# Kernel tuning notes

Measured on AMD Instinct MI355X. Metric: run time of the kernel, lower is better.

## Reference

```python
import jax, jax.numpy as jnp
import numpy as np

R = 8          # num_real
P = 8          # num_complex_conjugate_pairs
L = 4          # num_layers (hidden Linear+ReLU blocks)
H = 256        # hidden_dim
B = 16384      # batch


def _init_params(key, C, out_dim):
    ks = jax.random.split(key, 6)
    s_in = 1.0  # fan_in = 1
    s_h = 1.0 / np.sqrt(H)
    return dict(
        W_in=jax.random.uniform(ks[0], (C, H), jnp.float32, -s_in, s_in),
        b_in=jax.random.uniform(ks[1], (C, H), jnp.float32, -s_in, s_in),
        W_h=jax.random.uniform(ks[2], (L, C, H, H), jnp.float32, -s_h, s_h),
        b_h=jax.random.uniform(ks[3], (L, C, H), jnp.float32, -s_h, s_h),
        W_out=jax.random.uniform(ks[4], (C, out_dim, H), jnp.float32, -s_h, s_h),
        b_out=jax.random.uniform(ks[5], (C, out_dim), jnp.float32, -s_h, s_h),
    )


def setup_inputs() -> dict:
    key = jax.random.key(0)
    kz, kr, kc = jax.random.split(key, 3)
    z = jax.random.normal(kz, (B, R + 2 * P), jnp.float32)
    pr = _init_params(kr, R, 1)   # real-eigenvalue MLPs, out_dim=1
    pc = _init_params(kc, P, 2)   # complex-pair MLPs, out_dim=2
    return {
        "z": z,
        "Wr_in": pr["W_in"], "br_in": pr["b_in"],
        "Wr_h": pr["W_h"], "br_h": pr["b_h"],
        "Wr_out": pr["W_out"], "br_out": pr["b_out"],
        "Wc_in": pc["W_in"], "bc_in": pc["b_in"],
        "Wc_h": pc["W_h"], "bc_h": pc["b_h"],
        "Wc_out": pc["W_out"], "bc_out": pc["b_out"],
    }


def _grouped_mlp(x, W_in, b_in, W_h, b_h, W_out, b_out):
    # x: [B, C] scalar input per channel; all C tiny MLPs run as grouped GEMMs.
    h = jax.nn.relu(x[..., None] * W_in + b_in)            # [B, C, H]
    for l in range(W_h.shape[0]):
        h = jax.nn.relu(jnp.einsum('bci,coi->bco', h, W_h[l]) + b_h[l])
    return jnp.einsum('bci,coi->bco', h, W_out) + b_out     # [B, C, out]


def reference(z, Wr_in, br_in, Wr_h, br_h, Wr_out, br_out,
              Wc_in, bc_in, Wc_h, bc_h, Wc_out, bc_out):
    # real channels: z[..., i] -> Linear chains -> real_lambda [B, R]
    real_lambda = _grouped_mlp(z[..., :R], Wr_in, br_in, Wr_h, br_h,
                               Wr_out, br_out)[..., 0]
    # complex pairs: magnitude z_r^2 + z_i^2 per pair -> (mu, omega)
    z_mag = z[..., R::2] ** 2 + z[..., R + 1::2] ** 2        # [B, P]
    mu_omega = _grouped_mlp(z_mag, Wc_in, bc_in, Wc_h, bc_h,
                            Wc_out, bc_out)                  # [B, P, 2]
    mu = mu_omega[..., 0]
    omega = mu_omega[..., 1]
    return real_lambda, mu, omega
```

## Files before the change

### kernel.cpp

```cpp
#include <hip/hip_runtime.h>

#define OUT_MU 131072
#define OUT_OM 262144
#define WOUT_OFF 4210688

typedef _Float16 half8 __attribute__((ext_vector_type(8)));
typedef __fp16   fp16x2 __attribute__((ext_vector_type(2)));
typedef float    floatx4 __attribute__((ext_vector_type(4)));
typedef unsigned uint2v __attribute__((ext_vector_type(2)));

__device__ __forceinline__ void wait_lgkm0() {
    asm volatile("s_waitcnt lgkmcnt(0)" ::: "memory");
}
__device__ __forceinline__ void wait_vm0() {
    asm volatile("s_waitcnt vmcnt(0)" ::: "memory");
}
__device__ __forceinline__ void barrier_raw() {
    asm volatile("s_barrier" ::: "memory");
}

#define AS1 __attribute__((address_space(1)))
#define AS3 __attribute__((address_space(3)))

__global__ void prep_w(const float* __restrict__ Wr_h,
                       const float* __restrict__ Wc_h,
                       _Float16* __restrict__ dst) {
    int v = blockIdx.x * 256 + threadIdx.x;
    int r16 = v & 15;
    int ks  = (v >> 4) & 3;
    int nt  = (v >> 6) & 3;
    int wv  = (v >> 8) & 3;
    int g   = (v >> 10) & 31;
    int ch  = v >> 15;
    int l = g >> 3, kk = g & 7;
    int n  = wv * 64 + nt * 16 + r16;
    int k0 = kk * 32 + ks * 8;
    const float* src = (ch < 8) ? Wr_h : Wc_h;
    int c = ch & 7;
    const float* p = src + ((size_t)((l * 8 + c) * 256 + n)) * 256 + k0;
    float4 a = *(const float4*)p;
    float4 b = *(const float4*)(p + 4);
    half8 o;
    o[0] = (_Float16)a.x; o[1] = (_Float16)a.y; o[2] = (_Float16)a.z; o[3] = (_Float16)a.w;
    o[4] = (_Float16)b.x; o[5] = (_Float16)b.y; o[6] = (_Float16)b.z; o[7] = (_Float16)b.w;
    *(half8*)(dst + (size_t)v * 8) = o;
}

__global__ void prep_wo(const float* __restrict__ Wr_out,
                        const float* __restrict__ Wc_out,
                        _Float16* __restrict__ dst) {
    int t = blockIdx.x * 256 + threadIdx.x;
    int j = t & 255, d = (t >> 8) & 1, ch = t >> 9;
    int c = ch & 7;
    float v;
    if (ch < 8) v = d ? 0.f : Wr_out[c * 256 + j];
    else        v = Wc_out[(c * 2 + d) * 256 + j];
    dst[WOUT_OFF + t] = (_Float16)v;
}

__global__ __launch_bounds__(256, 2)
void mlp_fused(const float* __restrict__ z,
               const float* __restrict__ Wr_in, const float* __restrict__ br_in,
               const float* __restrict__ Wc_in, const float* __restrict__ bc_in,
               const float* __restrict__ br_h,  const float* __restrict__ bc_h,
               const float* __restrict__ br_out, const float* __restrict__ bc_out,
               const _Float16* __restrict__ wst,
               float* __restrict__ out) {
    __shared__ __align__(16) char smem[77824];
    const int tid  = threadIdx.x;
    const int lane = tid & 63;
    const int wv   = tid >> 6;
    const int bid  = blockIdx.x;
    const int ch   = bid & 15;
    const int m0   = (bid >> 4) * 128;
    const bool isC = ch >= 8;
    const int c    = ch & 7;
    const int ks   = lane >> 4;
    const int r16  = lane & 15;
    float* zbuf = (float*)(smem + 65536);

    {
        const float* zs = z + (size_t)m0 * 24 + wv * 768 + lane * 4;
        char* zd = smem + 65536 + wv * 3072;
        __builtin_amdgcn_global_load_lds((const AS1 void*)zs,         (AS3 void*)zd,          16, 0, 0);
        __builtin_amdgcn_global_load_lds((const AS1 void*)(zs + 256), (AS3 void*)(zd + 1024), 16, 0, 0);
        __builtin_amdgcn_global_load_lds((const AS1 void*)(zs + 512), (AS3 void*)(zd + 2048), 16, 0, 0);
    }

    const half8* wl = (const half8*)wst + (size_t)ch * 32768 + wv * 256 + lane;

    half8 wr2[2][4];
    #pragma unroll
    for (int nt = 0; nt < 4; ++nt) wr2[0][nt] = wl[nt * 64];

    const float* bh = (isC ? bc_h : br_h) + c * 256 + wv * 64 + ks * 4;

    const int vbase = r16 * 512 + (((r16 & 7) ^ ks) << 4);

    const int jg = tid & 31;
    const int rg = tid >> 5;
    const float* Wi = (isC ? Wc_in : Wr_in) + c * 256 + jg * 8;
    const float* bi = (isC ? bc_in : br_in) + c * 256 + jg * 8;
    float4 w0 = *(const float4*)Wi;
    float4 w1 = *(const float4*)(Wi + 4);
    float4 v0 = *(const float4*)bi;
    float4 v1 = *(const float4*)(bi + 4);

    wait_vm0();
    barrier_raw();

    {
        #pragma unroll
        for (int i = 0; i < 16; ++i) {
            int m = rg * 16 + i;
            float x;
            if (!isC) x = zbuf[m * 24 + c];
            else {
                float2 p = *(const float2*)(zbuf + m * 24 + 8 + 2 * c);
                x = p.x * p.x + p.y * p.y;
            }
            half8 o;
            o[0] = (_Float16)fmaxf(fmaf(x, w0.x, v0.x), 0.f);
            o[1] = (_Float16)fmaxf(fmaf(x, w0.y, v0.y), 0.f);
            o[2] = (_Float16)fmaxf(fmaf(x, w0.z, v0.z), 0.f);
            o[3] = (_Float16)fmaxf(fmaf(x, w0.w, v0.w), 0.f);
            o[4] = (_Float16)fmaxf(fmaf(x, w1.x, v1.x), 0.f);
            o[5] = (_Float16)fmaxf(fmaf(x, w1.y, v1.y), 0.f);
            o[6] = (_Float16)fmaxf(fmaf(x, w1.z, v1.z), 0.f);
            o[7] = (_Float16)fmaxf(fmaf(x, w1.w, v1.w), 0.f);
            *(half8*)(smem + m * 512 + ((jg ^ (m & 7)) << 4)) = o;
        }
    }
    wait_lgkm0();
    barrier_raw();

    #pragma unroll 1
    for (int l = 0; l < 4; ++l) {
        float4 bnt[4];
        #pragma unroll
        for (int nt = 0; nt < 4; ++nt)
            bnt[nt] = *(const float4*)(bh + l * 2048 + nt * 16);

        floatx4 acc[4][8];
        #pragma unroll
        for (int nt = 0; nt < 4; ++nt) {
            floatx4 bi4;
            bi4[0] = bnt[nt].x; bi4[1] = bnt[nt].y;
            bi4[2] = bnt[nt].z; bi4[3] = bnt[nt].w;
            #pragma unroll
            for (int mt = 0; mt < 8; ++mt) acc[nt][mt] = bi4;
        }

        half8 bfr[3][4];
        {
            const char* b0 = smem + vbase;
            #pragma unroll
            for (int j = 0; j < 4; ++j) bfr[0][j] = *(const half8*)(b0 + j * 8192);
            #pragma unroll
            for (int j = 0; j < 4; ++j) bfr[1][j] = *(const half8*)(b0 + 32768 + j * 8192);
        }

        #pragma unroll
        for (int hs = 0; hs < 16; ++hs) {
            const int kk = hs >> 1, half = hs & 1;
            if (half == 0) {
                const half8* p = wl + (size_t)(kk + 1) * 1024;
                #pragma unroll
                for (int nt = 0; nt < 4; ++nt) wr2[(kk + 1) & 1][nt] = p[nt * 64];
            }
            if (hs < 14) {
                const int nhs = hs + 2;
                const char* nb = smem + (vbase ^ ((nhs >> 1) << 6)) + (nhs & 1) * 32768;
                #pragma unroll
                for (int j = 0; j < 4; ++j)
                    bfr[nhs % 3][j] = *(const half8*)(nb + j * 8192);
            }
            __builtin_amdgcn_s_setprio(1);
            #pragma unroll
            for (int nt = 0; nt < 4; ++nt)
                #pragma unroll
                for (int j = 0; j < 4; ++j)
                    acc[nt][half * 4 + j] = __builtin_amdgcn_mfma_f32_16x16x32_f16(
                        wr2[kk & 1][nt], bfr[hs % 3][j], acc[nt][half * 4 + j], 0, 0, 0);
            __builtin_amdgcn_s_setprio(0);
        }
        wl += 8192;

        wait_lgkm0();
        barrier_raw();
        #pragma unroll
        for (int nt = 0; nt < 4; ++nt) {
            const int nb = wv * 64 + nt * 16 + ks * 4;
            const int sw = ((nb >> 3) << 4);
            #pragma unroll
            for (int mt = 0; mt < 8; ++mt) {
                const int m = mt * 16 + r16;
                floatx4 v = acc[nt][mt];
                union { fp16x2 h; unsigned u; } c0, c1;
                c0.h = __builtin_amdgcn_cvt_pkrtz(fmaxf(v[0], 0.f), fmaxf(v[1], 0.f));
                c1.h = __builtin_amdgcn_cvt_pkrtz(fmaxf(v[2], 0.f), fmaxf(v[3], 0.f));
                uint2v o; o[0] = c0.u; o[1] = c1.u;
                *(uint2v*)(smem + m * 512 + (sw ^ ((m & 7) << 4)) + (nb & 7) * 2) = o;
            }
        }
        wait_lgkm0();
        barrier_raw();
    }

    {
        const int q = tid & 1, m = tid >> 1;
        const half8* Wo = (const half8*)(wst + WOUT_OFF) + ch * 64 + q * 16;
        float s0 = 0.f, s1 = 0.f;
        #pragma unroll
        for (int i = 0; i < 16; ++i) {
            int slot = q * 16 + i;
            half8 hv = *(const half8*)(smem + m * 512 + ((slot ^ (m & 7)) << 4));
            half8 wo0 = Wo[i];
            #pragma unroll
            for (int e = 0; e < 8; ++e) s0 = fmaf((float)hv[e], (float)wo0[e], s0);
            if (isC) {
                half8 wo1 = Wo[32 + i];
                #pragma unroll
                for (int e = 0; e < 8; ++e) s1 = fmaf((float)hv[e], (float)wo1[e], s1);
            }
        }
        s0 += __shfl_xor(s0, 1);
        if (isC) s1 += __shfl_xor(s1, 1);
        if (q == 0) {
            const int row = m0 + m;
            if (!isC) {
                out[row * 8 + c] = s0 + br_out[c];
            } else {
                out[OUT_MU + row * 8 + c] = s0 + bc_out[c * 2];
                out[OUT_OM + row * 8 + c] = s1 + bc_out[c * 2 + 1];
            }
        }
    }
}

extern "C" void kernel_launch(void* const* d_in, const int* in_sizes, int n_in,
                              void* d_out, int out_size, void* d_ws, size_t ws_size,
                              hipStream_t stream) {
    const float* z      = (const float*)d_in[0];
    const float* Wr_in  = (const float*)d_in[1];
    const float* br_in  = (const float*)d_in[2];
    const float* Wr_h   = (const float*)d_in[3];
    const float* br_h   = (const float*)d_in[4];
    const float* Wr_out = (const float*)d_in[5];
    const float* br_out = (const float*)d_in[6];
    const float* Wc_in  = (const float*)d_in[7];
    const float* bc_in  = (const float*)d_in[8];
    const float* Wc_h   = (const float*)d_in[9];
    const float* bc_h   = (const float*)d_in[10];
    const float* Wc_out = (const float*)d_in[11];
    const float* bc_out = (const float*)d_in[12];
    _Float16* wst = (_Float16*)d_ws;
    float* out = (float*)d_out;

    prep_w<<<2048, 256, 0, stream>>>(Wr_h, Wc_h, wst);
    prep_wo<<<32, 256, 0, stream>>>(Wr_out, Wc_out, wst);
    mlp_fused<<<2048, 256, 0, stream>>>(z, Wr_in, br_in, Wc_in, bc_in,
                                        br_h, bc_h, br_out, bc_out, wst, out);
}
```

Baseline: 133.8 us.

## Split each layer into two row halves and overlap epilogue with MFMA

```diff
diff --git a/kernel.cpp b/kernel.cpp
--- a/kernel.cpp
+++ b/kernel.cpp
@@ -58,6 +58,79 @@
     dst[WOUT_OFF + t] = (_Float16)v;
 }
 
+template<int HALF, int EPIHALF, bool DO_EPI>
+__device__ __forceinline__ void run_phase(char* __restrict__ smem, int vbase,
+        const half8* __restrict__ wlg, const half8* __restrict__ wlg_next,
+        const float* __restrict__ bh_epi,
+        half8 (&wreg)[2][4],
+        floatx4 (&acc)[4][4], floatx4 (&eacc)[4][4],
+        int wv, int ks, int r16) {
+    float4 eb[4];
+    if (DO_EPI) {
+        #pragma unroll
+        for (int nt = 0; nt < 4; ++nt) eb[nt] = *(const float4*)(bh_epi + nt * 16);
+    }
+    #pragma unroll
+    for (int a = 0; a < 4; ++a)
+        #pragma unroll
+        for (int b = 0; b < 4; ++b) acc[a][b] = 0.f;
+
+    const int hb = HALF * 32768;
+    half8 bfr[2][4];
+    #pragma unroll
+    for (int j = 0; j < 4; ++j)
+        bfr[0][j] = *(const half8*)(smem + vbase + hb + j * 8192);
+
+    #pragma unroll
+    for (int kk = 0; kk < 8; ++kk) {
+        {
+            const half8* wp = (kk < 7 ? wlg : wlg_next) + ((kk + 1) & 7) * 1024;
+            #pragma unroll
+            for (int nt = 0; nt < 4; ++nt) wreg[(kk + 1) & 1][nt] = wp[nt * 64];
+        }
+        if (kk < 7) {
+            const char* nbp = smem + ((vbase ^ ((kk + 1) << 6)) + hb);
+            #pragma unroll
+            for (int j = 0; j < 4; ++j)
+                bfr[(kk + 1) & 1][j] = *(const half8*)(nbp + j * 8192);
+        }
+        __builtin_amdgcn_s_setprio(1);
+        #pragma unroll
+        for (int nt = 0; nt < 2; ++nt)
+            #pragma unroll
+            for (int mt = 0; mt < 4; ++mt)
+                acc[nt][mt] = __builtin_amdgcn_mfma_f32_16x16x32_f16(
+                    wreg[kk & 1][nt], bfr[kk & 1][mt], acc[nt][mt], 0, 0, 0);
+        __builtin_amdgcn_s_setprio(0);
+        if (DO_EPI) {
+            #pragma unroll
+            for (int c2 = 0; c2 < 2; ++c2) {
+                const int u = 2 * kk + c2, nt = u >> 2, mt = u & 3;
+                floatx4 v = eacc[nt][mt];
+                float4 b = eb[nt];
+                union { fp16x2 h; unsigned u32; } c0, c1;
+                c0.h = __builtin_amdgcn_cvt_pkrtz(fmaxf(v[0] + b.x, 0.f),
+                                                  fmaxf(v[1] + b.y, 0.f));
+                c1.h = __builtin_amdgcn_cvt_pkrtz(fmaxf(v[2] + b.z, 0.f),
+                                                  fmaxf(v[3] + b.w, 0.f));
+                const int nb = wv * 64 + nt * 16 + ks * 4;
+                const int m = EPIHALF * 64 + mt * 16 + r16;
+                uint2v o; o[0] = c0.u32; o[1] = c1.u32;
+                *(uint2v*)(smem + m * 512 + (((nb >> 3) << 4) ^ ((r16 & 7) << 4))
+                           + (nb & 7) * 2) = o;
+            }
+        }
+        __builtin_amdgcn_s_setprio(1);
+        #pragma unroll
+        for (int nt = 2; nt < 4; ++nt)
+            #pragma unroll
+            for (int mt = 0; mt < 4; ++mt)
+                acc[nt][mt] = __builtin_amdgcn_mfma_f32_16x16x32_f16(
+                    wreg[kk & 1][nt], bfr[kk & 1][mt], acc[nt][mt], 0, 0, 0);
+        __builtin_amdgcn_s_setprio(0);
+    }
+}
+
 __global__ __launch_bounds__(256, 2)
 void mlp_fused(const float* __restrict__ z,
                const float* __restrict__ Wr_in, const float* __restrict__ br_in,
@@ -87,11 +160,11 @@
         __builtin_amdgcn_global_load_lds((const AS1 void*)(zs + 512), (AS3 void*)(zd + 2048), 16, 0, 0);
     }
 
-    const half8* wl = (const half8*)wst + (size_t)ch * 32768 + wv * 256 + lane;
-
-    half8 wr2[2][4];
+    const half8* wlch = (const half8*)wst + (size_t)ch * 32768 + wv * 256 + lane;
+
+    half8 wreg[2][4];
     #pragma unroll
-    for (int nt = 0; nt < 4; ++nt) wr2[0][nt] = wl[nt * 64];
+    for (int nt = 0; nt < 4; ++nt) wreg[0][nt] = wlch[nt * 64];
 
     const float* bh = (isC ? bc_h : br_h) + c * 256 + wv * 64 + ks * 4;
 
@@ -134,78 +207,48 @@
     wait_lgkm0();
     barrier_raw();
 
+    floatx4 accA[4][4], accB[4][4];
+
+    run_phase<0, 1, false>(smem, vbase, wlch, wlch, bh,
+                           wreg, accA, accB, wv, ks, r16);
+    wait_lgkm0();
+    barrier_raw();
+
     #pragma unroll 1
     for (int l = 0; l < 4; ++l) {
-        float4 bnt[4];
-        #pragma unroll
-        for (int nt = 0; nt < 4; ++nt)
-            bnt[nt] = *(const float4*)(bh + l * 2048 + nt * 16);
-
-        floatx4 acc[4][8];
-        #pragma unroll
-        for (int nt = 0; nt < 4; ++nt) {
-            floatx4 bi4;
-            bi4[0] = bnt[nt].x; bi4[1] = bnt[nt].y;
-            bi4[2] = bnt[nt].z; bi4[3] = bnt[nt].w;
-            #pragma unroll
-            for (int mt = 0; mt < 8; ++mt) acc[nt][mt] = bi4;
-        }
-
-        half8 bfr[3][4];
-        {
-            const char* b0 = smem + vbase;
-            #pragma unroll
-            for (int j = 0; j < 4; ++j) bfr[0][j] = *(const half8*)(b0 + j * 8192);
-            #pragma unroll
-            for (int j = 0; j < 4; ++j) bfr[1][j] = *(const half8*)(b0 + 32768 + j * 8192);
-        }
-
-        #pragma unroll
-        for (int hs = 0; hs < 16; ++hs) {
-            const int kk = hs >> 1, half = hs & 1;
-            if (half == 0) {
-                const half8* p = wl + (size_t)(kk + 1) * 1024;
-                #pragma unroll
-                for (int nt = 0; nt < 4; ++nt) wr2[(kk + 1) & 1][nt] = p[nt * 64];
-            }
-            if (hs < 14) {
-                const int nhs = hs + 2;
-                const char* nb = smem + (vbase ^ ((nhs >> 1) << 6)) + (nhs & 1) * 32768;
-                #pragma unroll
-                for (int j = 0; j < 4; ++j)
-                    bfr[nhs % 3][j] = *(const half8*)(nb + j * 8192);
-            }
-            __builtin_amdgcn_s_setprio(1);
-            #pragma unroll
-            for (int nt = 0; nt < 4; ++nt)
-                #pragma unroll
-                for (int j = 0; j < 4; ++j)
-                    acc[nt][half * 4 + j] = __builtin_amdgcn_mfma_f32_16x16x32_f16(
-                        wr2[kk & 1][nt], bfr[hs % 3][j], acc[nt][half * 4 + j], 0, 0, 0);
-            __builtin_amdgcn_s_setprio(0);
-        }
-        wl += 8192;
-
+        const half8* wl_l = wlch + l * 8192;
+        run_phase<1, 0, true>(smem, vbase, wl_l, (l < 3 ? wl_l + 8192 : wl_l),
+                              bh + l * 2048, wreg, accB, accA, wv, ks, r16);
         wait_lgkm0();
         barrier_raw();
-        #pragma unroll
-        for (int nt = 0; nt < 4; ++nt) {
+        if (l < 3) {
+            run_phase<0, 1, true>(smem, vbase, wl_l + 8192, wl_l + 8192,
+                                  bh + l * 2048, wreg, accA, accB, wv, ks, r16);
+            wait_lgkm0();
+            barrier_raw();
+        }
+    }
+
+    {
+        float4 eb[4];
+        #pragma unroll
+        for (int nt = 0; nt < 4; ++nt) eb[nt] = *(const float4*)(bh + 3 * 2048 + nt * 16);
+        #pragma unroll
+        for (int u = 0; u < 16; ++u) {
+            const int nt = u >> 2, mt = u & 3;
+            floatx4 v = accB[nt][mt];
+            float4 b = eb[nt];
+            union { fp16x2 h; unsigned u32; } c0, c1;
+            c0.h = __builtin_amdgcn_cvt_pkrtz(fmaxf(v[0] + b.x, 0.f), fmaxf(v[1] + b.y, 0.f));
+            c1.h = __builtin_amdgcn_cvt_pkrtz(fmaxf(v[2] + b.z, 0.f), fmaxf(v[3] + b.w, 0.f));
             const int nb = wv * 64 + nt * 16 + ks * 4;
-            const int sw = ((nb >> 3) << 4);
-            #pragma unroll
-            for (int mt = 0; mt < 8; ++mt) {
-                const int m = mt * 16 + r16;
-                floatx4 v = acc[nt][mt];
-                union { fp16x2 h; unsigned u; } c0, c1;
-                c0.h = __builtin_amdgcn_cvt_pkrtz(fmaxf(v[0], 0.f), fmaxf(v[1], 0.f));
-                c1.h = __builtin_amdgcn_cvt_pkrtz(fmaxf(v[2], 0.f), fmaxf(v[3], 0.f));
-                uint2v o; o[0] = c0.u; o[1] = c1.u;
-                *(uint2v*)(smem + m * 512 + (sw ^ ((m & 7) << 4)) + (nb & 7) * 2) = o;
-            }
-        }
-        wait_lgkm0();
-        barrier_raw();
-    }
+            const int m = 64 + mt * 16 + r16;
+            uint2v o; o[0] = c0.u32; o[1] = c1.u32;
+            *(uint2v*)(smem + m * 512 + (((nb >> 3) << 4) ^ ((r16 & 7) << 4)) + (nb & 7) * 2) = o;
+        }
+    }
+    wait_lgkm0();
+    barrier_raw();
 
     {
         const int q = tid & 1, m = tid >> 1;
```

New measurement: 147.5 us. 10.2% more time.
